# Optimization experiments

Measured on AMD Instinct MI355X. Metric: run time of the kernel, lower is better.

Reference implementation:

```python
import jax, jax.numpy as jnp
import numpy as np

B, A, N, L = 4, 16, 8, 512
DE, DH, H, C = 256, 64, 8, 1.0
DHEAD = DE // H
LN_EPS = 1e-5

def _layernorm(x, w, b):
    mu = jnp.mean(x, axis=-1, keepdims=True)
    var = jnp.mean((x - mu) ** 2, axis=-1, keepdims=True)
    return (x - mu) / jnp.sqrt(var + LN_EPS) * w + b

def _logmap0(x, c):
    sc = jnp.sqrt(c)
    n = jnp.maximum(jnp.linalg.norm(x, axis=-1, keepdims=True), 1e-15)
    u = jnp.minimum(sc * n, 1.0 - 1e-5)  # stay inside artanh domain
    return jnp.arctanh(u) * x / (sc * n)

def _expmap0(u, c):
    sc = jnp.sqrt(c)
    n = jnp.maximum(jnp.linalg.norm(u, axis=-1, keepdims=True), 1e-15)
    return jnp.tanh(sc * n) * u / (sc * n)

def setup_inputs() -> dict:
    key = jax.random.key(0)
    ks = jax.random.split(key, 5)
    curr_rho = jax.random.normal(ks[0], (B, A, DE), jnp.float32)
    demo_rho = jax.random.normal(ks[1], (B, N, L, A, DE), jnp.float32)
    demo_hyp = jax.random.normal(ks[2], (B, N, L, DH), jnp.float32)
    # project hyperbolic points inside the unit Poincare ball
    demo_hyp = demo_hyp / (1.0 + jnp.linalg.norm(demo_hyp, axis=-1, keepdims=True)) * 0.9
    demo_mask = jnp.ones((B, N, L), jnp.int32)
    Wq = jax.random.normal(ks[3], (DE, DE), jnp.float32) / np.sqrt(DE)
    Wk = jax.random.normal(ks[4], (DE, DE), jnp.float32) / np.sqrt(DE)
    return {"curr_rho": curr_rho, "demo_rho": demo_rho, "demo_hyp": demo_hyp,
            "demo_mask": demo_mask, "Wq": Wq, "Wk": Wk,
            "ln_q_w": jnp.ones((DE,), jnp.float32), "ln_q_b": jnp.zeros((DE,), jnp.float32),
            "ln_k_w": jnp.ones((DE,), jnp.float32), "ln_k_b": jnp.zeros((DE,), jnp.float32)}

def reference(curr_rho, demo_rho, demo_hyp, demo_mask, Wq, Wk, ln_q_w, ln_q_b, ln_k_w, ln_k_b):
    # queries: [B,H,A,dh]
    q = (_layernorm(curr_rho, ln_q_w, ln_q_b) @ Wq.T).reshape(B, A, H, DHEAD).transpose(0, 2, 1, 3)
    # keys: [B,N,L,A,H,dh]; the original gather over agents with arange(A) is identity,
    # so scores align query agent a with key agent a directly.
    k = (_layernorm(demo_rho, ln_k_w, ln_k_b) @ Wk.T).reshape(B, N, L, A, H, DHEAD)
    scores = jnp.einsum('bhad,bnlahd->bhanl', q, k) / np.sqrt(DHEAD)  # [B,H,A,N,L]
    dm = demo_mask[:, None, None, :, :]
    scores = jnp.where(dm == 0, -jnp.inf, scores)
    attn_flat = jax.nn.softmax(scores.reshape(B, H, A, N * L), axis=-1)
    # Poincare weighted mean in tangent space at origin
    vals_tan0 = _logmap0(demo_hyp.reshape(B, N * L, DH), C)          # [B,NL,dh_h]
    m_h = jnp.einsum('bhax,bxd->bhad', attn_flat, vals_tan0)          # [B,H,A,d_h]
    y_h_tan0 = _logmap0(_expmap0(m_h, C), C)
    curr_hyp = _expmap0(jnp.mean(y_h_tan0, axis=1), C)                # [B,A,d_h]
    max_rad = 1.0 / np.sqrt(C) - 1e-5
    norm = jnp.maximum(jnp.linalg.norm(curr_hyp, axis=-1, keepdims=True), 1e-6)
    curr_hyp = curr_hyp * jnp.minimum(max_rad / norm, 1.0)
    curr_hyp = jnp.mean(curr_hyp, axis=1)                             # [B,d_h] (as in source)
    return curr_hyp, attn_flat.reshape(B, H, A, N, L)
```

## Files before the change

kernel.cpp:

```cpp
#include <hip/hip_runtime.h>
#include <math.h>

#define LN_EPS_ 1e-5f
#define INV_SQRT_DHEAD 0.17677669529663687f


__device__ __forceinline__ float waveReduceSum(float v) {
    #pragma unroll
    for (int m = 32; m > 0; m >>= 1) v += __shfl_xor(v, m, 64);
    return v;
}
__device__ __forceinline__ float waveReduceMax(float v) {
    #pragma unroll
    for (int m = 32; m > 0; m >>= 1) v = fmaxf(v, __shfl_xor(v, m, 64));
    return v;
}

__global__ __launch_bounds__(256) void k_prep(
    const float* __restrict__ curr_rho, const float* __restrict__ Wq,
    const float* __restrict__ Wk, const float* __restrict__ lnqw,
    const float* __restrict__ lnqb, const float* __restrict__ lnkw,
    const float* __restrict__ lnkb,
    float* __restrict__ g, float* __restrict__ s0, float* __restrict__ s2)
{
    __shared__ float xs[256];
    __shared__ float qs[256];
    __shared__ float red[8];
    const int t = threadIdx.x;
    const int w = t >> 6;
    const int ba = blockIdx.x;
    const float x = curr_rho[(size_t)ba * 256 + t];

    float sm = waveReduceSum(x);
    if ((t & 63) == 0) red[w] = sm;
    __syncthreads();
    const float mu = (red[0] + red[1] + red[2] + red[3]) * (1.0f / 256.0f);
    __syncthreads();
    const float dx = x - mu;
    float sq = waveReduceSum(dx * dx);
    if ((t & 63) == 0) red[w] = sq;
    __syncthreads();
    const float var = (red[0] + red[1] + red[2] + red[3]) * (1.0f / 256.0f);
    const float rstd = 1.0f / sqrtf(var + LN_EPS_);
    __syncthreads();
    xs[t] = dx * rstd * lnqw[t] + lnqb[t];
    __syncthreads();

    {
        const float4* wq4 = (const float4*)(Wq + (size_t)t * 256);
        float acc = 0.f;
        #pragma unroll 8
        for (int e4 = 0; e4 < 64; ++e4) {
            float4 wv = wq4[e4];
            acc += xs[e4*4+0]*wv.x + xs[e4*4+1]*wv.y + xs[e4*4+2]*wv.z + xs[e4*4+3]*wv.w;
        }
        qs[t] = acc;
    }
    __syncthreads();

    for (int h = 0; h < 8; ++h) {
        float qk = 0.f;
        #pragma unroll 8
        for (int dh = 0; dh < 32; ++dh)
            qk += qs[h*32+dh] * Wk[(size_t)(h*32+dh)*256 + t];
        const float gv = lnkw[t] * qk;
        const float b2 = lnkb[t] * qk;
        g[((size_t)ba * 8 + h) * 256 + t] = gv;
        float sg = waveReduceSum(gv);
        float sb = waveReduceSum(b2);
        if ((t & 63) == 0) { red[w] = sg; red[4 + w] = sb; }
        __syncthreads();
        if (t == 0) {
            s0[ba*8+h] = red[0] + red[1] + red[2] + red[3];
            s2[ba*8+h] = red[4] + red[5] + red[6] + red[7];
        }
        __syncthreads();
    }
}

__global__ __launch_bounds__(256) void k_vals(
    const float* __restrict__ demo_hyp, float* __restrict__ vals)
{
    const int t = threadIdx.x;
    const size_t idx = (size_t)blockIdx.x * 256 + t;
    const float x = demo_hyp[idx];
    const float ss = waveReduceSum(x * x);
    const float nrm = sqrtf(ss);
    const float n = fmaxf(nrm, 1e-15f);
    const float u = fminf(n, 1.0f - 1e-5f);
    const float f = atanhf(u) / n;
    vals[idx] = x * f;
}

__global__ __launch_bounds__(256) void k_scores(
    const float* __restrict__ demo_rho, const int* __restrict__ demo_mask,
    const float* __restrict__ g, const float* __restrict__ s0,
    const float* __restrict__ s2, float* __restrict__ attn)
{
    __shared__ float sbuf[8][132];
    const int t = threadIdx.x;
    const int gid = blockIdx.x;
    const int lc = gid & 3;
    const int n  = (gid >> 2) & 7;
    const int a  = (gid >> 5) & 15;
    const int b  = gid >> 9;
    const int c  = t & 31;
    const int r  = t >> 5;

    float gr[8][8];
    {
        const float* gb = g + ((size_t)(b*16 + a) * 8) * 256 + c * 8;
        #pragma unroll
        for (int h = 0; h < 8; ++h) {
            float4 ga = *(const float4*)(gb + h * 256);
            float4 gc = *(const float4*)(gb + h * 256 + 4);
            gr[h][0]=ga.x; gr[h][1]=ga.y; gr[h][2]=ga.z; gr[h][3]=ga.w;
            gr[h][4]=gc.x; gr[h][5]=gc.y; gr[h][6]=gc.z; gr[h][7]=gc.w;
        }
    }
    const float s0v = s0[(b*16 + a) * 8 + (c & 7)];
    const float s2v = s2[(b*16 + a) * 8 + (c & 7)];
    const int* mrow = demo_mask + (b*8 + n) * 512 + lc * 128;

    const float* xbase = demo_rho +
        ((size_t)((b*8 + n) * 512 + lc * 128) * 16 + a) * 256 + c * 8;

    #pragma unroll 2
    for (int p = 0; p < 16; ++p) {
        const float* xp = xbase + (size_t)(p * 8 + r) * 4096;
        float4 xa = *(const float4*)(xp);
        float4 xb = *(const float4*)(xp + 4);
        float xv[8] = {xa.x, xa.y, xa.z, xa.w, xb.x, xb.y, xb.z, xb.w};

        float v[10];
        #pragma unroll
        for (int h = 0; h < 8; ++h) {
            float acc = 0.f;
            #pragma unroll
            for (int j = 0; j < 8; ++j) acc += xv[j] * gr[h][j];
            v[h] = acc;
        }
        float sm = 0.f, sq = 0.f;
        #pragma unroll
        for (int j = 0; j < 8; ++j) { sm += xv[j]; sq += xv[j] * xv[j]; }
        v[8] = sm; v[9] = sq;

        #pragma unroll
        for (int m = 1; m <= 16; m <<= 1) {
            #pragma unroll
            for (int i = 0; i < 10; ++i) v[i] += __shfl_xor(v[i], m, 32);
        }

        if (c < 8) {
            const float mu   = v[8] * (1.0f / 256.0f);
            const float var  = v[9] * (1.0f / 256.0f) - mu * mu;
            const float rstd = 1.0f / sqrtf(var + LN_EPS_);
            float sc = (rstd * (v[c] - mu * s0v) + s2v) * INV_SQRT_DHEAD;
            const int lidx = p * 8 + r;
            if (mrow[lidx] == 0) sc = -INFINITY;
            sbuf[c][lidx] = sc;
        }
    }
    __syncthreads();
    {
        const int h = t >> 5;
        const float* rowp = &sbuf[h][0];
        float4 vout = *(const float4*)(rowp + c * 4);
        const size_t off = (size_t)((b*8 + h) * 16 + a) * 4096 + n * 512 + lc * 128 + c * 4;
        *(float4*)(attn + off) = vout;
    }
}

__global__ __launch_bounds__(256) void k_softmax_mh(
    float* __restrict__ attn, const float* __restrict__ vals,
    float* __restrict__ mh)
{
    __shared__ float p0[4096];
    __shared__ float p1[4096];
    __shared__ float red[4];
    __shared__ float mpart[4][64];
    const int t = threadIdx.x;
    const int w = t >> 6;
    const int row0 = blockIdx.x * 2;
    const int b = row0 >> 7;

    for (int rr = 0; rr < 2; ++rr) {
        const int row = row0 + rr;
        float* dst = attn + (size_t)row * 4096;
        float* pl = rr ? p1 : p0;
        float lmax = -INFINITY;
        float4 v4[4];
        #pragma unroll
        for (int k = 0; k < 4; ++k) {
            float4 vv = ((const float4*)dst)[k * 256 + t];
            v4[k] = vv;
            lmax = fmaxf(lmax, fmaxf(fmaxf(vv.x, vv.y), fmaxf(vv.z, vv.w)));
        }
        lmax = waveReduceMax(lmax);
        if ((t & 63) == 0) red[w] = lmax;
        __syncthreads();
        const float mx = fmaxf(fmaxf(red[0], red[1]), fmaxf(red[2], red[3]));
        __syncthreads();
        float lsum = 0.f;
        #pragma unroll
        for (int k = 0; k < 4; ++k) {
            float4 vv = v4[k];
            vv.x = __expf(vv.x - mx); vv.y = __expf(vv.y - mx);
            vv.z = __expf(vv.z - mx); vv.w = __expf(vv.w - mx);
            v4[k] = vv;
            lsum += vv.x + vv.y + vv.z + vv.w;
        }
        lsum = waveReduceSum(lsum);
        if ((t & 63) == 0) red[w] = lsum;
        __syncthreads();
        const float inv = 1.0f / (red[0] + red[1] + red[2] + red[3]);
        __syncthreads();
        #pragma unroll
        for (int k = 0; k < 4; ++k) {
            float4 vv = v4[k];
            vv.x *= inv; vv.y *= inv; vv.z *= inv; vv.w *= inv;
            ((float4*)pl)[k * 256 + t] = vv;
            ((float4*)dst)[k * 256 + t] = vv;
        }
    }
    __syncthreads();

    const int ch = t >> 6, d = t & 63;
    const float* vb = vals + (size_t)b * 4096 * 64 + d;
    float acc0a = 0.f, acc0b = 0.f, acc1a = 0.f, acc1b = 0.f;
    const int x0 = ch * 1024;
    #pragma unroll 16
    for (int x = x0; x < x0 + 1024; x += 2) {
        const float va = vb[(size_t)x * 64];
        const float vc = vb[(size_t)(x + 1) * 64];
        acc0a += p0[x] * va;     acc0b += p0[x + 1] * vc;
        acc1a += p1[x] * va;     acc1b += p1[x + 1] * vc;
    }
    const float acc0 = acc0a + acc0b;
    const float acc1 = acc1a + acc1b;
    for (int rr = 0; rr < 2; ++rr) {
        mpart[ch][d] = rr ? acc1 : acc0;
        __syncthreads();
        if (t < 64) {
            const float m = mpart[0][t] + mpart[1][t] + mpart[2][t] + mpart[3][t];
            mh[(size_t)(row0 + rr) * 64 + t] = m;
        }
        __syncthreads();
    }
}

__global__ __launch_bounds__(1024) void k_final(
    const float* __restrict__ mh, float* __restrict__ out)
{
    __shared__ float contrib[16][64];
    const int t = threadIdx.x;
    const int a = t >> 6, d = t & 63;
    const int b = blockIdx.x;
    float accY = 0.f;
    #pragma unroll
    for (int h = 0; h < 8; ++h) {
        const float m = mh[(size_t)((b*8 + h) * 16 + a) * 64 + d];
        const float ss = waveReduceSum(m * m);
        const float nm = sqrtf(ss);
        const float n1 = fmaxf(nm, 1e-15f);
        const float t1 = tanhf(n1);
        const float e  = t1 * m / n1;
        const float ne = t1 * nm / n1;
        const float n2 = fmaxf(ne, 1e-15f);
        const float u  = fminf(n2, 1.0f - 1e-5f);
        accY += atanhf(u) * e / n2;
    }
    const float ym = accY * 0.125f;
    const float ssy = waveReduceSum(ym * ym);
    const float nmy = sqrtf(ssy);
    const float n3 = fmaxf(nmy, 1e-15f);
    const float t3 = tanhf(n3);
    const float chv = t3 * ym / n3;
    const float nch = t3 * nmy / n3;
    const float nrm = fmaxf(nch, 1e-6f);
    const float sc = fminf((1.0f - 1e-5f) / nrm, 1.0f);
    contrib[a][d] = chv * sc;
    __syncthreads();
    if (t < 64) {
        float s = 0.f;
        #pragma unroll
        for (int a2 = 0; a2 < 16; ++a2) s += contrib[a2][t];
        out[b * 64 + t] = s * (1.0f / 16.0f);
    }
}

extern "C" void kernel_launch(void* const* d_in, const int* in_sizes, int n_in,
                              void* d_out, int out_size, void* d_ws, size_t ws_size,
                              hipStream_t stream) {
    const float* curr_rho  = (const float*)d_in[0];
    const float* demo_rho  = (const float*)d_in[1];
    const float* demo_hyp  = (const float*)d_in[2];
    const int*   demo_mask = (const int*)d_in[3];
    const float* Wq   = (const float*)d_in[4];
    const float* Wk   = (const float*)d_in[5];
    const float* lnqw = (const float*)d_in[6];
    const float* lnqb = (const float*)d_in[7];
    const float* lnkw = (const float*)d_in[8];
    const float* lnkb = (const float*)d_in[9];

    float* out  = (float*)d_out;
    float* attn = out + 256;

    float* ws   = (float*)d_ws;
    float* g    = ws;
    float* s0   = ws + 131072;
    float* s2   = ws + 131584;
    float* vals = ws + 132096;
    float* mh   = ws + 1180672;

    hipLaunchKernelGGL(k_prep, dim3(64), dim3(256), 0, stream,
                       curr_rho, Wq, Wk, lnqw, lnqb, lnkw, lnkb, g, s0, s2);
    hipLaunchKernelGGL(k_vals, dim3(4096), dim3(256), 0, stream, demo_hyp, vals);
    hipLaunchKernelGGL(k_scores, dim3(2048), dim3(256), 0, stream,
                       demo_rho, demo_mask, g, s0, s2, attn);
    hipLaunchKernelGGL(k_softmax_mh, dim3(256), dim3(256), 0, stream, attn, vals, mh);
    hipLaunchKernelGGL(k_final, dim3(4), dim3(1024), 0, stream, mh, out);
}
```

Before: 457.6 us.

## Use transpose-reduce shuffles in scores and split softmax rows across 512 threads

In k_scores, the 10 independent butterfly shuffle reductions are replaced with a recursive-halving transpose reduction. Each lane ends up owning one reduced value, and the LN sum and sum-of-squares are broadcast with two extra shuffles, which cuts the shuffle count substantially. k_softmax_mh now launches 512 threads so both attention rows get their softmax computed in parallel by separate halves instead of one after the other. The weighted sum over vals is then split across 8 waves instead of 4, with a single-pass final reduction. This raises per-block parallelism and cuts serialized barriers, at the cost of more LDS for the partial sums and a larger block size.

Measured after the change: 445.9 us. -2.5%, faster.

```diff
diff --git a/kernel.cpp b/kernel.cpp
--- a/kernel.cpp
+++ b/kernel.cpp
@@ -145,17 +145,36 @@
         for (int j = 0; j < 8; ++j) { sm += xv[j]; sq += xv[j] * xv[j]; }
         v[8] = sm; v[9] = sq;
 
-        #pragma unroll
-        for (int m = 1; m <= 16; m <<= 1) {
-            #pragma unroll
-            for (int i = 0; i < 10; ++i) v[i] += __shfl_xor(v[i], m, 32);
-        }
+        const int lb0 = c & 1, lb1 = c & 2, lb2 = c & 4, lb3 = c & 8;
+        float a0 = lb0 ? v[1] : v[0]; float q0 = lb0 ? v[0] : v[1];
+        a0 += __shfl_xor(q0, 1, 32);
+        float a1 = lb0 ? v[3] : v[2]; float q1 = lb0 ? v[2] : v[3];
+        a1 += __shfl_xor(q1, 1, 32);
+        float a2 = lb0 ? v[5] : v[4]; float q2 = lb0 ? v[4] : v[5];
+        a2 += __shfl_xor(q2, 1, 32);
+        float a3 = lb0 ? v[7] : v[6]; float q3 = lb0 ? v[6] : v[7];
+        a3 += __shfl_xor(q3, 1, 32);
+        float a4 = lb0 ? v[9] : v[8]; float q4 = lb0 ? v[8] : v[9];
+        a4 += __shfl_xor(q4, 1, 32);
+        float w0 = lb1 ? a1 : a0; float r0 = lb1 ? a0 : a1;
+        w0 += __shfl_xor(r0, 2, 32);
+        float w1 = lb1 ? a3 : a2; float r1 = lb1 ? a2 : a3;
+        w1 += __shfl_xor(r1, 2, 32);
+        float w2 = a4 + __shfl_xor(a4, 2, 32);
+        float x0 = lb2 ? w1 : w0; float r2 = lb2 ? w0 : w1;
+        x0 += __shfl_xor(r2, 4, 32);
+        float x1 = w2 + __shfl_xor(w2, 4, 32);
+        float y = lb3 ? x1 : x0; float r3 = lb3 ? x0 : x1;
+        y += __shfl_xor(r3, 8, 32);
+        y += __shfl_xor(y, 16, 32);
+        const float smv = __shfl(y, 8, 32);
+        const float sqv = __shfl(y, 9, 32);
 
         if (c < 8) {
-            const float mu   = v[8] * (1.0f / 256.0f);
-            const float var  = v[9] * (1.0f / 256.0f) - mu * mu;
+            const float mu   = smv * (1.0f / 256.0f);
+            const float var  = sqv * (1.0f / 256.0f) - mu * mu;
             const float rstd = 1.0f / sqrtf(var + LN_EPS_);
-            float sc = (rstd * (v[c] - mu * s0v) + s2v) * INV_SQRT_DHEAD;
+            float sc = (rstd * (y - mu * s0v) + s2v) * INV_SQRT_DHEAD;
             const int lidx = p * 8 + r;
             if (mrow[lidx] == 0) sc = -INFINITY;
             sbuf[c][lidx] = sc;
@@ -171,81 +190,82 @@
     }
 }
 
-__global__ __launch_bounds__(256) void k_softmax_mh(
+__global__ __launch_bounds__(512) void k_softmax_mh(
     float* __restrict__ attn, const float* __restrict__ vals,
     float* __restrict__ mh)
 {
     __shared__ float p0[4096];
     __shared__ float p1[4096];
-    __shared__ float red[4];
-    __shared__ float mpart[4][64];
-    const int t = threadIdx.x;
-    const int w = t >> 6;
+    __shared__ float red[2][4];
+    __shared__ float mpart[2][8][64];
+    const int t = threadIdx.x;
+    const int half = t >> 8;
+    const int tt = t & 255;
+    const int w = tt >> 6;
     const int row0 = blockIdx.x * 2;
+    const int row = row0 + half;
     const int b = row0 >> 7;
 
-    for (int rr = 0; rr < 2; ++rr) {
-        const int row = row0 + rr;
-        float* dst = attn + (size_t)row * 4096;
-        float* pl = rr ? p1 : p0;
-        float lmax = -INFINITY;
-        float4 v4[4];
-        #pragma unroll
-        for (int k = 0; k < 4; ++k) {
-            float4 vv = ((const float4*)dst)[k * 256 + t];
-            v4[k] = vv;
-            lmax = fmaxf(lmax, fmaxf(fmaxf(vv.x, vv.y), fmaxf(vv.z, vv.w)));
-        }
-        lmax = waveReduceMax(lmax);
-        if ((t & 63) == 0) red[w] = lmax;
-        __syncthreads();
-        const float mx = fmaxf(fmaxf(red[0], red[1]), fmaxf(red[2], red[3]));
-        __syncthreads();
-        float lsum = 0.f;
-        #pragma unroll
-        for (int k = 0; k < 4; ++k) {
-            float4 vv = v4[k];
-            vv.x = __expf(vv.x - mx); vv.y = __expf(vv.y - mx);
-            vv.z = __expf(vv.z - mx); vv.w = __expf(vv.w - mx);
-            v4[k] = vv;
-            lsum += vv.x + vv.y + vv.z + vv.w;
-        }
-        lsum = waveReduceSum(lsum);
-        if ((t & 63) == 0) red[w] = lsum;
-        __syncthreads();
-        const float inv = 1.0f / (red[0] + red[1] + red[2] + red[3]);
-        __syncthreads();
-        #pragma unroll
-        for (int k = 0; k < 4; ++k) {
-            float4 vv = v4[k];
-            vv.x *= inv; vv.y *= inv; vv.z *= inv; vv.w *= inv;
-            ((float4*)pl)[k * 256 + t] = vv;
-            ((float4*)dst)[k * 256 + t] = vv;
-        }
+    float* dst = attn + (size_t)row * 4096;
+    float* pl = half ? p1 : p0;
+
+    float lmax = -INFINITY;
+    float4 v4[4];
+    #pragma unroll
+    for (int k = 0; k < 4; ++k) {
+        float4 vv = ((const float4*)dst)[k * 256 + tt];
+        v4[k] = vv;
+        lmax = fmaxf(lmax, fmaxf(fmaxf(vv.x, vv.y), fmaxf(vv.z, vv.w)));
+    }
+    lmax = waveReduceMax(lmax);
+    if ((tt & 63) == 0) red[half][w] = lmax;
+    __syncthreads();
+    const float mx = fmaxf(fmaxf(red[half][0], red[half][1]),
+                           fmaxf(red[half][2], red[half][3]));
+    __syncthreads();
+    float lsum = 0.f;
+    #pragma unroll
+    for (int k = 0; k < 4; ++k) {
+        float4 vv = v4[k];
+        vv.x = __expf(vv.x - mx); vv.y = __expf(vv.y - mx);
+        vv.z = __expf(vv.z - mx); vv.w = __expf(vv.w - mx);
+        v4[k] = vv;
+        lsum += vv.x + vv.y + vv.z + vv.w;
+    }
+    lsum = waveReduceSum(lsum);
+    if ((tt & 63) == 0) red[half][w] = lsum;
+    __syncthreads();
+    const float inv = 1.0f / (red[half][0] + red[half][1] +
+                              red[half][2] + red[half][3]);
+    #pragma unroll
+    for (int k = 0; k < 4; ++k) {
+        float4 vv = v4[k];
+        vv.x *= inv; vv.y *= inv; vv.z *= inv; vv.w *= inv;
+        ((float4*)pl)[k * 256 + tt] = vv;
+        ((float4*)dst)[k * 256 + tt] = vv;
     }
     __syncthreads();
 
     const int ch = t >> 6, d = t & 63;
-    const float* vb = vals + (size_t)b * 4096 * 64 + d;
+    const float* vb = vals + (size_t)b * 262144 + d;
     float acc0a = 0.f, acc0b = 0.f, acc1a = 0.f, acc1b = 0.f;
-    const int x0 = ch * 1024;
+    const int x0 = ch * 512;
     #pragma unroll 16
-    for (int x = x0; x < x0 + 1024; x += 2) {
+    for (int x = x0; x < x0 + 512; x += 2) {
         const float va = vb[(size_t)x * 64];
         const float vc = vb[(size_t)(x + 1) * 64];
         acc0a += p0[x] * va;     acc0b += p0[x + 1] * vc;
         acc1a += p1[x] * va;     acc1b += p1[x + 1] * vc;
     }
-    const float acc0 = acc0a + acc0b;
-    const float acc1 = acc1a + acc1b;
-    for (int rr = 0; rr < 2; ++rr) {
-        mpart[ch][d] = rr ? acc1 : acc0;
-        __syncthreads();
-        if (t < 64) {
-            const float m = mpart[0][t] + mpart[1][t] + mpart[2][t] + mpart[3][t];
-            mh[(size_t)(row0 + rr) * 64 + t] = m;
-        }
-        __syncthreads();
+    mpart[0][ch][d] = acc0a + acc0b;
+    mpart[1][ch][d] = acc1a + acc1b;
+    __syncthreads();
+    if (t < 128) {
+        const int rr = t >> 6, dd = t & 63;
+        float s = 0.f;
+        #pragma unroll
+        for (int cc = 0; cc < 8; ++cc) s += mpart[rr][cc][dd];
+        mh[(size_t)(row0 + rr) * 64 + dd] = s;
     }
 }
 
@@ -318,6 +338,6 @@
     hipLaunchKernelGGL(k_vals, dim3(4096), dim3(256), 0, stream, demo_hyp, vals);
     hipLaunchKernelGGL(k_scores, dim3(2048), dim3(256), 0, stream,
                        demo_rho, demo_mask, g, s0, s2, attn);
-    hipLaunchKernelGGL(k_softmax_mh, dim3(256), dim3(256), 0, stream, attn, vals, mh);
+    hipLaunchKernelGGL(k_softmax_mh, dim3(256), dim3(512), 0, stream, attn, vals, mh);
     hipLaunchKernelGGL(k_final, dim3(4), dim3(1024), 0, stream, mh, out);
 }
```
